# Performance work log

Hardware: AMD Instinct MI355X
Metric: run time of the kernel (lower is better)

Reference implementation:

```python
import jax, jax.numpy as jnp
import numpy as np

IN_DIM = 64
OUT_DIM = 16  # SPD matrix side
HIDDEN = [128, 128]
CHOL_DIM = OUT_DIM + OUT_DIM * (OUT_DIM - 1) // 2  # 136
BATCH = 65536
LEAKY_SLOPE = 0.01  # torch.nn.LeakyReLU default


def _uniform(key, shape, in_feat):
    b = 1.0 / in_feat
    return jax.random.uniform(key, shape, jnp.float32, -b, b)


def setup_inputs() -> dict:
    key = jax.random.key(0)
    ks = jax.random.split(key, 7)
    x = jax.random.normal(ks[0], (BATCH, IN_DIM), jnp.float32)
    # layer sizes: 64 -> 128 -> 128 -> 136, init uniform(-1/in_feat, 1/in_feat)
    W1 = _uniform(ks[1], (IN_DIM, HIDDEN[0]), IN_DIM)
    b1 = _uniform(ks[2], (HIDDEN[0],), IN_DIM)
    W2 = _uniform(ks[3], (HIDDEN[0], HIDDEN[1]), HIDDEN[0])
    b2 = _uniform(ks[4], (HIDDEN[1],), HIDDEN[0])
    W3 = _uniform(ks[5], (HIDDEN[1], CHOL_DIM), HIDDEN[1])
    b3 = _uniform(ks[6], (CHOL_DIM,), HIDDEN[1])
    return {"x": x, "W1": W1, "b1": b1, "W2": W2, "b2": b2, "W3": W3, "b3": b3}


def reference(x, W1, b1, W2, b2, W3, b3):
    # MLP with LeakyReLU between layers, then Tanh on final output
    h = jax.nn.leaky_relu(x @ W1 + b1, LEAKY_SLOPE)
    h = jax.nn.leaky_relu(h @ W2 + b2, LEAKY_SLOPE)
    ldata = jnp.tanh(h @ W3 + b3)  # [B, 136]

    # fill_tril: scatter the 136 values into the lower triangle (row-major)
    rows, cols = jnp.tril_indices(OUT_DIM)
    L = jnp.zeros((x.shape[0], OUT_DIM, OUT_DIM), x.dtype).at[:, rows, cols].set(ldata)
    Q = L + jnp.swapaxes(L, -1, -2)  # symmetric [B, 16, 16]

    # symmetric eigendecomposition (ascending eigenvalues, like torch.symeig)
    w, V = jnp.linalg.eigh(Q)
    # sqrt(softmax(exp(w)**2)) ; exp(w)**2 == exp(2w)
    ev = jnp.sqrt(jax.nn.softmax(jnp.exp(2.0 * w), axis=-1))  # [B, 16]
    # faithful to source: uses inverse (== V^T in exact math since V orthogonal)
    Vinv = jnp.linalg.inv(V)
    # V @ diag(ev) @ V^{-1}
    return jnp.einsum('bij,bj,bjk->bik', V, ev, Vinv)
```

## Files before the change

kernel.cpp:

```cpp
#include <hip/hip_runtime.h>
#include <math.h>

typedef _Float16 f16;
typedef _Float16 half4_t __attribute__((ext_vector_type(4)));
typedef _Float16 half8_t __attribute__((ext_vector_type(8)));
typedef float floatx4 __attribute__((ext_vector_type(4)));

__global__ __launch_bounds__(256) void prep_weights(
    const float* __restrict__ W1, const float* __restrict__ W2,
    const float* __restrict__ W3, f16* __restrict__ wt) {
  int t = blockIdx.x * 256 + threadIdx.x;
  if (t < 8192) {
    int c = t >> 6, k = t & 63;
    wt[t] = (f16)W1[k * 128 + c];
  } else if (t < 24576) {
    int u = t - 8192;
    int c = u >> 7, k = u & 127;
    wt[t] = (f16)W2[k * 128 + c];
  } else if (t < 43008) {
    int u = t - 24576;
    int c = u >> 7, k = u & 127;
    wt[t] = (f16)((c < 136) ? W3[k * 136 + c] : 0.0f);
  }
}

__device__ __forceinline__ float fast_tanh(float v) {
  float e = __builtin_amdgcn_exp2f(v * 2.885390081777926814f);
  return 1.0f - 2.0f * __builtin_amdgcn_rcpf(e + 1.0f);
}

template <int CTRL>
__device__ __forceinline__ float dpp_add(float v) {
  int t = __builtin_amdgcn_update_dpp(0, __builtin_bit_cast(int, v), CTRL,
                                      0xf, 0xf, true);
  return v + __builtin_bit_cast(float, t);
}
__device__ __forceinline__ float wsum(float v) {
  v = dpp_add<0x111>(v);
  v = dpp_add<0x112>(v);
  v = dpp_add<0x114>(v);
  v = dpp_add<0x118>(v);
  v = dpp_add<0x142>(v);
  v = dpp_add<0x143>(v);
  return __builtin_bit_cast(
      float, __builtin_amdgcn_readlane(__builtin_bit_cast(int, v), 63));
}

__device__ __forceinline__ half4_t to_h(floatx4 v) {
  auto p0 = __builtin_amdgcn_cvt_pkrtz(v[0], v[1]);
  auto p1 = __builtin_amdgcn_cvt_pkrtz(v[2], v[3]);
  half4_t h;
  h[0] = p0[0]; h[1] = p0[1]; h[2] = p1[0]; h[3] = p1[1];
  return h;
}

__device__ __forceinline__ floatx4 expm_c(floatx4 b, floatx4 I4, float& m) {
  float s2 = wsum(b[0] * b[0] + b[1] * b[1] + b[2] * b[2] + b[3] * b[3]);
  float td = wsum(I4[0] * b[0] + I4[1] * b[1] + I4[2] * b[2] + I4[3] * b[3]);
  m = td * 0.0625f;
  float fr2 = fmaxf(s2 - td * m, 1e-30f);
  int e2 = (int)(__builtin_bit_cast(unsigned, fr2) >> 23) - 127;
  int s = (e2 + 5) >> 1;
  s = s < 0 ? 0 : (s > 12 ? 12 : s);
  s = __builtin_amdgcn_readfirstlane(s);
  float sc = __builtin_bit_cast(float, (unsigned)(127 - s) << 23);
  b = (b - I4 * m) * sc;
  half4_t bh = to_h(b);
  floatx4 zero = {0.f, 0.f, 0.f, 0.f};
  floatx4 a2 = __builtin_amdgcn_mfma_f32_16x16x16f16(bh, bh, zero, 0, 0, 0);
  floatx4 t = I4 * 0.5f + b * (1.f / 6.f) + a2 * (1.f / 24.f);
  floatx4 p = __builtin_amdgcn_mfma_f32_16x16x16f16(to_h(a2), to_h(t), I4 + b,
                                                    0, 0, 0);
  for (int k = 0; k < s; ++k) {
    half4_t ph = to_h(p);
    p = __builtin_amdgcn_mfma_f32_16x16x16f16(ph, ph, zero, 0, 0, 0);
  }
  return p;
}

__global__ __launch_bounds__(256, 4) void fused_kernel(
    const float* __restrict__ x, const float* __restrict__ b1,
    const float* __restrict__ b2v, const float* __restrict__ b3,
    const f16* __restrict__ wt, float* __restrict__ out) {
  __shared__ f16 act1[2048];
  __shared__ f16 act2[2048];
  __shared__ f16 lds_ld[32 * 144];

  const int lane = threadIdx.x & 63;
  const int w = threadIdx.x >> 6;
  const int cl = lane & 15;
  const int q = lane >> 4;
  const f16* w1t = wt;
  const f16* w2t = wt + 8192;
  const f16* w3t = wt + 24576;

  half8_t w2f[2][4];
  float bias1[2], bias2[2], bias3[3];
#pragma unroll
  for (int j = 0; j < 2; ++j) {
    int c8g = w + 4 * j;
    int c = c8g * 16 + cl;
#pragma unroll
    for (int ks = 0; ks < 4; ++ks)
      w2f[j][ks] = *(const half8_t*)(w2t + c * 128 + ks * 32 + q * 8);
    bias1[j] = b1[c];
    bias2[j] = b2v[c];
  }
#pragma unroll
  for (int j = 0; j < 3; ++j) {
    int cc = (w + 4 * j) * 16 + cl;
    bias3[j] = (cc < 136) ? b3[cc] : 0.f;
  }

  const int r0b = blockIdx.x * 32;
  const float* xp = x + (size_t)(r0b + cl) * 64 + q * 8;
  floatx4 v0 = *(const floatx4*)xp;
  floatx4 v1 = *(const floatx4*)(xp + 4);
  floatx4 v2 = *(const floatx4*)(xp + 32);
  floatx4 v3 = *(const floatx4*)(xp + 36);

  for (int t = 0; t < 2; ++t) {
    half8_t a0, a1;
#pragma unroll
    for (int i = 0; i < 4; ++i) {
      a0[i] = (f16)v0[i]; a0[i + 4] = (f16)v1[i];
      a1[i] = (f16)v2[i]; a1[i + 4] = (f16)v3[i];
    }
    if (t == 0) {
      xp = x + (size_t)(r0b + 16 + cl) * 64 + q * 8;
      v0 = *(const floatx4*)xp;
      v1 = *(const floatx4*)(xp + 4);
      v2 = *(const floatx4*)(xp + 32);
      v3 = *(const floatx4*)(xp + 36);
    }

#pragma unroll
    for (int j = 0; j < 2; ++j) {
      int c8g = w + 4 * j;
      int c = c8g * 16 + cl;
      half8_t u0 = *(const half8_t*)(w1t + c * 64 + q * 8);
      half8_t u1 = *(const half8_t*)(w1t + c * 64 + 32 + q * 8);
      floatx4 acc = {0.f, 0.f, 0.f, 0.f};
      acc = __builtin_amdgcn_mfma_f32_16x16x32_f16(a0, u0, acc, 0, 0, 0);
      acc = __builtin_amdgcn_mfma_f32_16x16x32_f16(a1, u1, acc, 0, 0, 0);
#pragma unroll
      for (int i = 0; i < 4; ++i) {
        float v = acc[i] + bias1[j];
        v = v > 0.f ? v : 0.01f * v;
        int row = q * 4 + i;
        int gs = ((c8g * 2 + (cl >> 3)) ^ row) & 15;
        act1[row * 128 + gs * 8 + (cl & 7)] = (f16)v;
      }
    }
    __syncthreads();

    half8_t ha[4];
#pragma unroll
    for (int ks = 0; ks < 4; ++ks)
      ha[ks] = *(const half8_t*)(act1 + cl * 128 +
                                 ((((ks << 2) | q) ^ cl) << 3));

#pragma unroll
    for (int j = 0; j < 2; ++j) {
      int c8g = w + 4 * j;
      floatx4 acc = {0.f, 0.f, 0.f, 0.f};
#pragma unroll
      for (int ks = 0; ks < 4; ++ks)
        acc = __builtin_amdgcn_mfma_f32_16x16x32_f16(ha[ks], w2f[j][ks], acc,
                                                     0, 0, 0);
#pragma unroll
      for (int i = 0; i < 4; ++i) {
        float v = acc[i] + bias2[j];
        v = v > 0.f ? v : 0.01f * v;
        int row = q * 4 + i;
        int gs = ((c8g * 2 + (cl >> 3)) ^ row) & 15;
        act2[row * 128 + gs * 8 + (cl & 7)] = (f16)v;
      }
    }
    __syncthreads();

#pragma unroll
    for (int ks = 0; ks < 4; ++ks)
      ha[ks] = *(const half8_t*)(act2 + cl * 128 +
                                 ((((ks << 2) | q) ^ cl) << 3));

#pragma unroll
    for (int j = 0; j < 3; ++j) {
      int c8g = w + 4 * j;
      if (c8g < 9) {
        int c = c8g * 16 + cl;
        floatx4 acc = {0.f, 0.f, 0.f, 0.f};
#pragma unroll
        for (int ks = 0; ks < 4; ++ks) {
          half8_t wv = *(const half8_t*)(w3t + c * 128 + ks * 32 + q * 8);
          acc = __builtin_amdgcn_mfma_f32_16x16x32_f16(ha[ks], wv, acc,
                                                       0, 0, 0);
        }
#pragma unroll
        for (int i = 0; i < 4; ++i) {
          float v = fast_tanh(acc[i] + bias3[j]);
          lds_ld[(t * 16 + q * 4 + i) * 144 + c] = (f16)v;
        }
      }
    }
  }
  __syncthreads();

  const int r = cl;
#pragma unroll 2
  for (int jj = 0; jj < 8; ++jj) {
    int m_loc = w * 8 + jj;
    const f16* ld = lds_ld + m_loc * 144;

    floatx4 b, I4;
#pragma unroll
    for (int i = 0; i < 4; ++i) {
      int k = q * 4 + i;
      int hi = r > k ? r : k;
      int lo = r + k - hi;
      float v = (float)ld[hi * (hi + 1) / 2 + lo];
      bool d = (r == k);
      I4[i] = d ? 1.f : 0.f;
      b[i] = d ? 4.f * v : 2.f * v;
    }

    float m1;
    floatx4 p = expm_c(b, I4, m1);
    float fac = __builtin_amdgcn_exp2f(m1 * 1.4426950408889634f - 1.0f);
    float m2;
    p = expm_c(p * fac, I4, m2);

    float n2 = wsum(p[0] * p[0] + p[1] * p[1] + p[2] * p[2] + p[3] * p[3]);
    float inv = __builtin_amdgcn_rsqf(n2);
    floatx4 o = p * inv;
    size_t mat = (size_t)(r0b + m_loc);
    *(floatx4*)(out + mat * 256 + r * 16 + q * 4) = o;
  }
}

extern "C" void kernel_launch(void* const* d_in, const int* in_sizes, int n_in,
                              void* d_out, int out_size, void* d_ws,
                              size_t ws_size, hipStream_t stream) {
  const float* x = (const float*)d_in[0];
  const float* W1 = (const float*)d_in[1];
  const float* b1 = (const float*)d_in[2];
  const float* W2 = (const float*)d_in[3];
  const float* b2 = (const float*)d_in[4];
  const float* W3 = (const float*)d_in[5];
  const float* b3 = (const float*)d_in[6];
  float* out = (float*)d_out;
  f16* wt = (f16*)d_ws;

  prep_weights<<<168, 256, 0, stream>>>(W1, W2, W3, wt);
  fused_kernel<<<2048, 256, 0, stream>>>(x, b1, b2, b3, wt, out);
}
```

Baseline: 135.2 us.

## Use degree-8 Taylor expm with fewer squarings and widen blocks to 512 threads

The matrix exponential now uses a higher-order Taylor polynomial (through degree 8, built from b, b^2, b^3 and b^4 MFMAs). The scaling exponent is lowered by two, which removes about two squaring MFMAs per expm call, and there are two expm calls per matrix. Blocks grow to 8 waves handling 64 rows, so each wave owns one 16-column slice of every layer and keeps the W3 fragments in registers. This replaces the per-wave loops over column groups. The cost is extra MFMAs in the polynomial, a little more fp16 error risk from the larger scaled norm, and one wave doing extra work for the last 8 W3 columns.

```diff
diff --git a/kernel.cpp b/kernel.cpp
--- a/kernel.cpp
+++ b/kernel.cpp
@@ -54,13 +54,18 @@
   return h;
 }
 
-__device__ __forceinline__ floatx4 expm_c(floatx4 b, floatx4 I4, float& m) {
-  float s2 = wsum(b[0] * b[0] + b[1] * b[1] + b[2] * b[2] + b[3] * b[3]);
-  float td = wsum(I4[0] * b[0] + I4[1] * b[1] + I4[2] * b[2] + I4[3] * b[3]);
+__device__ __forceinline__ float dot4(floatx4 a, floatx4 b) {
+  return a[0] * b[0] + a[1] * b[1] + a[2] * b[2] + a[3] * b[3];
+}
+
+__device__ __forceinline__ floatx4 expm_c(floatx4 b, floatx4 I4, floatx4 i24,
+                                          float& m) {
+  float s2 = wsum(dot4(b, b));
+  float td = wsum(dot4(I4, b));
   m = td * 0.0625f;
   float fr2 = fmaxf(s2 - td * m, 1e-30f);
   int e2 = (int)(__builtin_bit_cast(unsigned, fr2) >> 23) - 127;
-  int s = (e2 + 5) >> 1;
+  int s = (e2 + 1) >> 1;
   s = s < 0 ? 0 : (s > 12 ? 12 : s);
   s = __builtin_amdgcn_readfirstlane(s);
   float sc = __builtin_bit_cast(float, (unsigned)(127 - s) << 23);
@@ -68,8 +73,24 @@
   half4_t bh = to_h(b);
   floatx4 zero = {0.f, 0.f, 0.f, 0.f};
   floatx4 a2 = __builtin_amdgcn_mfma_f32_16x16x16f16(bh, bh, zero, 0, 0, 0);
-  floatx4 t = I4 * 0.5f + b * (1.f / 6.f) + a2 * (1.f / 24.f);
-  floatx4 p = __builtin_amdgcn_mfma_f32_16x16x16f16(to_h(a2), to_h(t), I4 + b,
+  half4_t a2h = to_h(a2);
+  floatx4 b3 = __builtin_amdgcn_mfma_f32_16x16x16f16(a2h, bh, zero, 0, 0, 0);
+  floatx4 a4 = __builtin_amdgcn_mfma_f32_16x16x16f16(a2h, a2h, zero, 0, 0, 0);
+  floatx4 p0 = I4 + b;
+#pragma unroll
+  for (int i = 0; i < 4; ++i) {
+    p0[i] = fmaf(a2[i], 0.5f, p0[i]);
+    p0[i] = fmaf(b3[i], 1.f / 6.f, p0[i]);
+  }
+  floatx4 inner = i24;
+#pragma unroll
+  for (int i = 0; i < 4; ++i) {
+    inner[i] = fmaf(b[i], 1.f / 120.f, inner[i]);
+    inner[i] = fmaf(a2[i], 1.f / 720.f, inner[i]);
+    inner[i] = fmaf(b3[i], 1.f / 5040.f, inner[i]);
+    inner[i] = fmaf(a4[i], 1.f / 40320.f, inner[i]);
+  }
+  floatx4 p = __builtin_amdgcn_mfma_f32_16x16x16f16(to_h(a4), to_h(inner), p0,
                                                     0, 0, 0);
   for (int k = 0; k < s; ++k) {
     half4_t ph = to_h(p);
@@ -78,13 +99,13 @@
   return p;
 }
 
-__global__ __launch_bounds__(256, 4) void fused_kernel(
+__global__ __launch_bounds__(512, 4) void fused_kernel(
     const float* __restrict__ x, const float* __restrict__ b1,
     const float* __restrict__ b2v, const float* __restrict__ b3,
     const f16* __restrict__ wt, float* __restrict__ out) {
   __shared__ f16 act1[2048];
   __shared__ f16 act2[2048];
-  __shared__ f16 lds_ld[32 * 144];
+  __shared__ f16 lds_ld[64 * 144];
 
   const int lane = threadIdx.x & 63;
   const int w = threadIdx.x >> 6;
@@ -94,50 +115,36 @@
   const f16* w2t = wt + 8192;
   const f16* w3t = wt + 24576;
 
-  half8_t w2f[2][4];
-  float bias1[2], bias2[2], bias3[3];
-#pragma unroll
-  for (int j = 0; j < 2; ++j) {
-    int c8g = w + 4 * j;
-    int c = c8g * 16 + cl;
-#pragma unroll
-    for (int ks = 0; ks < 4; ++ks)
-      w2f[j][ks] = *(const half8_t*)(w2t + c * 128 + ks * 32 + q * 8);
-    bias1[j] = b1[c];
-    bias2[j] = b2v[c];
-  }
-#pragma unroll
-  for (int j = 0; j < 3; ++j) {
-    int cc = (w + 4 * j) * 16 + cl;
-    bias3[j] = (cc < 136) ? b3[cc] : 0.f;
-  }
-
-  const int r0b = blockIdx.x * 32;
-  const float* xp = x + (size_t)(r0b + cl) * 64 + q * 8;
-  floatx4 v0 = *(const floatx4*)xp;
-  floatx4 v1 = *(const floatx4*)(xp + 4);
-  floatx4 v2 = *(const floatx4*)(xp + 32);
-  floatx4 v3 = *(const floatx4*)(xp + 36);
-
-  for (int t = 0; t < 2; ++t) {
+  const int c = w * 16 + cl;
+
+  half8_t w2f[4], w3f[4];
+#pragma unroll
+  for (int ks = 0; ks < 4; ++ks) {
+    w2f[ks] = *(const half8_t*)(w2t + c * 128 + ks * 32 + q * 8);
+    w3f[ks] = *(const half8_t*)(w3t + c * 128 + ks * 32 + q * 8);
+  }
+  float bias1 = b1[c];
+  float bias2 = b2v[c];
+  float bias3 = b3[c];
+  float bias3x = (cl < 8) ? b3[128 + cl] : 0.f;
+
+  const int r0b = blockIdx.x * 64;
+
+  for (int t = 0; t < 4; ++t) {
+    const int r0 = r0b + t * 16;
+    const float* xp = x + (size_t)(r0 + cl) * 64 + q * 8;
+    floatx4 v0 = *(const floatx4*)xp;
+    floatx4 v1 = *(const floatx4*)(xp + 4);
+    floatx4 v2 = *(const floatx4*)(xp + 32);
+    floatx4 v3 = *(const floatx4*)(xp + 36);
     half8_t a0, a1;
 #pragma unroll
     for (int i = 0; i < 4; ++i) {
       a0[i] = (f16)v0[i]; a0[i + 4] = (f16)v1[i];
       a1[i] = (f16)v2[i]; a1[i + 4] = (f16)v3[i];
     }
-    if (t == 0) {
-      xp = x + (size_t)(r0b + 16 + cl) * 64 + q * 8;
-      v0 = *(const floatx4*)xp;
-      v1 = *(const floatx4*)(xp + 4);
-      v2 = *(const floatx4*)(xp + 32);
-      v3 = *(const floatx4*)(xp + 36);
-    }
-
-#pragma unroll
-    for (int j = 0; j < 2; ++j) {
-      int c8g = w + 4 * j;
-      int c = c8g * 16 + cl;
+
+    {
       half8_t u0 = *(const half8_t*)(w1t + c * 64 + q * 8);
       half8_t u1 = *(const half8_t*)(w1t + c * 64 + 32 + q * 8);
       floatx4 acc = {0.f, 0.f, 0.f, 0.f};
@@ -145,10 +152,10 @@
       acc = __builtin_amdgcn_mfma_f32_16x16x32_f16(a1, u1, acc, 0, 0, 0);
 #pragma unroll
       for (int i = 0; i < 4; ++i) {
-        float v = acc[i] + bias1[j];
+        float v = acc[i] + bias1;
         v = v > 0.f ? v : 0.01f * v;
         int row = q * 4 + i;
-        int gs = ((c8g * 2 + (cl >> 3)) ^ row) & 15;
+        int gs = ((w * 2 + (cl >> 3)) ^ row) & 15;
         act1[row * 128 + gs * 8 + (cl & 7)] = (f16)v;
       }
     }
@@ -160,20 +167,18 @@
       ha[ks] = *(const half8_t*)(act1 + cl * 128 +
                                  ((((ks << 2) | q) ^ cl) << 3));
 
-#pragma unroll
-    for (int j = 0; j < 2; ++j) {
-      int c8g = w + 4 * j;
+    {
       floatx4 acc = {0.f, 0.f, 0.f, 0.f};
 #pragma unroll
       for (int ks = 0; ks < 4; ++ks)
-        acc = __builtin_amdgcn_mfma_f32_16x16x32_f16(ha[ks], w2f[j][ks], acc,
+        acc = __builtin_amdgcn_mfma_f32_16x16x32_f16(ha[ks], w2f[ks], acc,
                                                      0, 0, 0);
 #pragma unroll
       for (int i = 0; i < 4; ++i) {
-        float v = acc[i] + bias2[j];
+        float v = acc[i] + bias2;
         v = v > 0.f ? v : 0.01f * v;
         int row = q * 4 + i;
-        int gs = ((c8g * 2 + (cl >> 3)) ^ row) & 15;
+        int gs = ((w * 2 + (cl >> 3)) ^ row) & 15;
         act2[row * 128 + gs * 8 + (cl & 7)] = (f16)v;
       }
     }
@@ -184,53 +189,65 @@
       ha[ks] = *(const half8_t*)(act2 + cl * 128 +
                                  ((((ks << 2) | q) ^ cl) << 3));
 
-#pragma unroll
-    for (int j = 0; j < 3; ++j) {
-      int c8g = w + 4 * j;
-      if (c8g < 9) {
-        int c = c8g * 16 + cl;
-        floatx4 acc = {0.f, 0.f, 0.f, 0.f};
-#pragma unroll
-        for (int ks = 0; ks < 4; ++ks) {
-          half8_t wv = *(const half8_t*)(w3t + c * 128 + ks * 32 + q * 8);
-          acc = __builtin_amdgcn_mfma_f32_16x16x32_f16(ha[ks], wv, acc,
-                                                       0, 0, 0);
-        }
-#pragma unroll
-        for (int i = 0; i < 4; ++i) {
-          float v = fast_tanh(acc[i] + bias3[j]);
-          lds_ld[(t * 16 + q * 4 + i) * 144 + c] = (f16)v;
-        }
+    {
+      floatx4 acc = {0.f, 0.f, 0.f, 0.f};
+#pragma unroll
+      for (int ks = 0; ks < 4; ++ks)
+        acc = __builtin_amdgcn_mfma_f32_16x16x32_f16(ha[ks], w3f[ks], acc,
+                                                     0, 0, 0);
+#pragma unroll
+      for (int i = 0; i < 4; ++i) {
+        float v = fast_tanh(acc[i] + bias3);
+        lds_ld[(t * 16 + q * 4 + i) * 144 + c] = (f16)v;
+      }
+    }
+    if (w == 0) {
+      int cx = 128 + cl;
+      floatx4 acc = {0.f, 0.f, 0.f, 0.f};
+#pragma unroll
+      for (int ks = 0; ks < 4; ++ks) {
+        half8_t wv = *(const half8_t*)(w3t + cx * 128 + ks * 32 + q * 8);
+        acc = __builtin_amdgcn_mfma_f32_16x16x32_f16(ha[ks], wv, acc, 0, 0, 0);
+      }
+#pragma unroll
+      for (int i = 0; i < 4; ++i) {
+        float v = fast_tanh(acc[i] + bias3x);
+        lds_ld[(t * 16 + q * 4 + i) * 144 + cx] = (f16)v;
       }
     }
   }
   __syncthreads();
 
   const int r = cl;
+  floatx4 I4, i24;
+#pragma unroll
+  for (int i = 0; i < 4; ++i) {
+    I4[i] = (r == q * 4 + i) ? 1.f : 0.f;
+    i24[i] = I4[i] * (1.f / 24.f);
+  }
+
 #pragma unroll 2
   for (int jj = 0; jj < 8; ++jj) {
     int m_loc = w * 8 + jj;
     const f16* ld = lds_ld + m_loc * 144;
 
-    floatx4 b, I4;
+    floatx4 b;
 #pragma unroll
     for (int i = 0; i < 4; ++i) {
       int k = q * 4 + i;
       int hi = r > k ? r : k;
       int lo = r + k - hi;
       float v = (float)ld[hi * (hi + 1) / 2 + lo];
-      bool d = (r == k);
-      I4[i] = d ? 1.f : 0.f;
-      b[i] = d ? 4.f * v : 2.f * v;
+      b[i] = (r == k) ? 4.f * v : 2.f * v;
     }
 
     float m1;
-    floatx4 p = expm_c(b, I4, m1);
+    floatx4 p = expm_c(b, I4, i24, m1);
     float fac = __builtin_amdgcn_exp2f(m1 * 1.4426950408889634f - 1.0f);
     float m2;
-    p = expm_c(p * fac, I4, m2);
-
-    float n2 = wsum(p[0] * p[0] + p[1] * p[1] + p[2] * p[2] + p[3] * p[3]);
+    p = expm_c(p * fac, I4, i24, m2);
+
+    float n2 = wsum(dot4(p, p));
     float inv = __builtin_amdgcn_rsqf(n2);
     floatx4 o = p * inv;
     size_t mat = (size_t)(r0b + m_loc);
@@ -252,5 +269,5 @@
   f16* wt = (f16*)d_ws;
 
   prep_weights<<<168, 256, 0, stream>>>(W1, W2, W3, wt);
-  fused_kernel<<<2048, 256, 0, stream>>>(x, b1, b2, b3, wt, out);
-}
+  fused_kernel<<<1024, 512, 0, stream>>>(x, b1, b2, b3, wt, out);
+}
```

After: 134.9 us. Within noise of the previous version (-0.2%).
